# Kernel tuning notes

Measured on AMD Instinct MI355X. Metric: run time of the kernel, lower is better.

## Reference

```python
import jax, jax.numpy as jnp
import numpy as np

B, N, QDIM = 2, 4096, 768
H, D = 8, 64  # num_head, head_dim; inner_dim = 512
INNER = H * D


def setup_inputs() -> dict:
    key = jax.random.key(0)
    ks = jax.random.split(key, 6)
    s = lambda fan_in: 1.0 / np.sqrt(fan_in)
    return {
        "x": jax.random.normal(ks[0], (B, N, QDIM), dtype=jnp.float32),
        "Wq": jax.random.normal(ks[1], (QDIM, INNER), dtype=jnp.float32) * s(QDIM),
        "Wk": jax.random.normal(ks[2], (QDIM, INNER), dtype=jnp.float32) * s(QDIM),
        "Wv": jax.random.normal(ks[3], (QDIM, INNER), dtype=jnp.float32) * s(QDIM),
        "Wout": jax.random.normal(ks[4], (INNER, QDIM), dtype=jnp.float32) * s(INNER),
        "b_out": jnp.zeros((QDIM,), dtype=jnp.float32),
    }


def reference(x, Wq, Wk, Wv, Wout, b_out):
    # x: [b, n, q_dim]; self-attention (kv = x), no mask, dropout = 0 (eval).
    scale = D ** -0.5
    # project and split heads: [b, n, h*d] -> [b, h, n, d]
    def heads(t):
        b, n, _ = t.shape
        return t.reshape(b, n, H, D).transpose(0, 2, 1, 3)
    q = heads(x @ Wq)
    k = heads(x @ Wk)
    v = heads(x @ Wv)
    qk = jnp.einsum("bhid,bhjd->bhij", q, k) * scale  # [b, h, n, n] -- O(n^2) matrix
    attn = jax.nn.softmax(qk, axis=-1)
    out = jnp.einsum("bhij,bhjd->bhid", attn, v)  # [b, h, n, d]
    out = out.transpose(0, 2, 1, 3).reshape(x.shape[0], x.shape[1], INNER)
    return out @ Wout + b_out
```

## Files before the change

kernel.cpp:

```cpp
#include <hip/hip_runtime.h>
#include <cstdint>
#include <cstddef>


typedef __attribute__((ext_vector_type(8))) short short8;
typedef __attribute__((ext_vector_type(4))) float f32x4;

__device__ __forceinline__ unsigned short f2bf(float f) {
  unsigned int u = __float_as_uint(f);
  u = (u + 0x7fffu + ((u >> 16) & 1u)) >> 16;
  return (unsigned short)u;
}

__device__ __forceinline__ float fast_exp2(float x) {
#if __has_builtin(__builtin_amdgcn_exp2f)
  return __builtin_amdgcn_exp2f(x);
#else
  return __expf(x * 0.69314718055994531f);
#endif
}

__device__ __forceinline__ void gld16(const void* g, void* l) {
  __builtin_amdgcn_global_load_lds(
      (__attribute__((address_space(1))) void*)const_cast<void*>(g),
      (__attribute__((address_space(3))) void*)l, 16, 0, 0);
}


__global__ __launch_bounds__(256) void cvt_x_k(const float* __restrict__ x,
                                               unsigned short* __restrict__ xb) {
  const size_t i = ((size_t)blockIdx.x * 256 + threadIdx.x) * 4;
  const float4 v = *(const float4*)(x + i);
  ushort4 u;
  u.x = f2bf(v.x); u.y = f2bf(v.y); u.z = f2bf(v.z); u.w = f2bf(v.w);
  *(ushort4*)(xb + i) = u;
}

__global__ __launch_bounds__(256) void transpose_w_k(
    const float* __restrict__ Wq, const float* __restrict__ Wk,
    const float* __restrict__ Wv, const float* __restrict__ Wout,
    unsigned short* __restrict__ Wt,
    unsigned short* __restrict__ WoT)
{
  __shared__ float t[32][33];
  const int z = blockIdx.z;
  const float* src = (z == 0) ? Wq : (z == 1) ? Wk : (z == 2) ? Wv : Wout;
  const int R = (z < 3) ? 768 : 512, C = (z < 3) ? 512 : 768;
  unsigned short* dst = (z < 3) ? (Wt + (size_t)z * 393216) : WoT;
  const int tx = threadIdx.x & 31, ty = threadIdx.x >> 5;
  const int c0 = blockIdx.x * 32, r0 = blockIdx.y * 32;
  if (c0 >= C || r0 >= R) return;
#pragma unroll
  for (int k = 0; k < 4; ++k)
    t[ty + 8 * k][tx] = src[(size_t)(r0 + ty + 8 * k) * C + c0 + tx];
  __syncthreads();
#pragma unroll
  for (int k = 0; k < 4; ++k)
    dst[(size_t)(c0 + ty + 8 * k) * R + r0 + tx] = f2bf(t[tx][ty + 8 * k]);
}


__global__ __launch_bounds__(256) void gemm_qkv_k(
    const unsigned short* __restrict__ A,
    const unsigned short* __restrict__ Wt,
    unsigned short* __restrict__ qb, unsigned short* __restrict__ kb,
    unsigned short* __restrict__ vtb) {
  __shared__ __align__(16) short Al[4096];
  __shared__ __align__(16) short Bl[4096];
  const int tid = threadIdx.x;
  const int w = tid >> 6, lane = tid & 63, quad = lane >> 4, l15 = lane & 15;
  const int wy = w >> 1, wx = w & 1;
  const int m0 = blockIdx.x * 128, n0 = blockIdx.y * 128;
  const int z = blockIdx.z;
  const unsigned short* Bt = Wt + (size_t)z * (512 * 768);

  f32x4 acc[4][4];
#pragma unroll
  for (int i = 0; i < 4; ++i)
#pragma unroll
    for (int j = 0; j < 4; ++j) acc[i][j] = (f32x4){0.f, 0.f, 0.f, 0.f};

  for (int k0 = 0; k0 < 768; k0 += 32) {
    __syncthreads();
#pragma unroll
    for (int s = 0; s < 2; ++s) {
      const int t = s * 256 + tid;
      gld16(A + (size_t)(m0 + (t >> 2)) * 768 + k0 + (t & 3) * 8,
            Al + s * 2048 + w * 512);
      gld16(Bt + (size_t)(n0 + (t >> 2)) * 768 + k0 + (t & 3) * 8,
            Bl + s * 2048 + w * 512);
    }
    __syncthreads();
    short8 af[4], bf[4];
#pragma unroll
    for (int i = 0; i < 4; ++i) {
      af[i] = *(const short8*)(Al + (wy * 64 + i * 16 + l15) * 32 + quad * 8);
      bf[i] = *(const short8*)(Bl + (wx * 64 + i * 16 + l15) * 32 + quad * 8);
    }
    if (z == 2) {
#pragma unroll
      for (int i = 0; i < 4; ++i)
#pragma unroll
        for (int j = 0; j < 4; ++j)
          acc[i][j] = __builtin_amdgcn_mfma_f32_16x16x32_bf16(af[i], bf[j], acc[i][j], 0, 0, 0);
    } else {
#pragma unroll
      for (int i = 0; i < 4; ++i)
#pragma unroll
        for (int j = 0; j < 4; ++j)
          acc[i][j] = __builtin_amdgcn_mfma_f32_16x16x32_bf16(bf[i], af[j], acc[i][j], 0, 0, 0);
    }
  }

  if (z == 2) {
#pragma unroll
    for (int i = 0; i < 4; ++i) {
#pragma unroll
      for (int j = 0; j < 4; ++j) {
        const int m0r = m0 + wy * 64 + i * 16 + quad * 4;
        const int n = n0 + wx * 64 + j * 16 + l15;
        const int b = m0r >> 12, nseq0 = m0r & 4095;
        const int h = n >> 6, d = n & 63;
        ushort4 u;
        u.x = f2bf(acc[i][j][0]); u.y = f2bf(acc[i][j][1]);
        u.z = f2bf(acc[i][j][2]); u.w = f2bf(acc[i][j][3]);
        *(ushort4*)(vtb + (size_t)((b * 8 + h) * 64 + d) * 4096 + nseq0) = u;
      }
    }
  } else {
    const float qs = 0.18033688011112042f;
#pragma unroll
    for (int i = 0; i < 4; ++i) {
#pragma unroll
      for (int j = 0; j < 4; ++j) {
        const int n0r = n0 + wx * 64 + i * 16 + quad * 4;
        const int m = m0 + wy * 64 + j * 16 + l15;
        const int b = m >> 12, nseq = m & 4095;
        const int h = n0r >> 6, d0 = n0r & 63;
        ushort4 u;
        if (z == 0) {
          u.x = f2bf(acc[i][j][0] * qs); u.y = f2bf(acc[i][j][1] * qs);
          u.z = f2bf(acc[i][j][2] * qs); u.w = f2bf(acc[i][j][3] * qs);
          *(ushort4*)(qb + (size_t)((b * 8 + h) * 4096 + nseq) * 64 + d0) = u;
        } else {
          u.x = f2bf(acc[i][j][0]); u.y = f2bf(acc[i][j][1]);
          u.z = f2bf(acc[i][j][2]); u.w = f2bf(acc[i][j][3]);
          *(ushort4*)(kb + (size_t)((b * 8 + h) * 4096 + nseq) * 64 + d0) = u;
        }
      }
    }
  }
}


__global__ __launch_bounds__(256) void attn_k(
    const unsigned short* __restrict__ qb,
    const unsigned short* __restrict__ kb,
    const unsigned short* __restrict__ vtb,
    unsigned short* __restrict__ ob) {
  __shared__ __align__(16) char smem[65536];
  short* Kl = (short*)smem;
  short* Vl = (short*)(smem + 16384);
  short* Pl = (short*)(smem + 32768);

  const int tid = threadIdx.x;
  const int w = tid >> 6, lane = tid & 63, quad = lane >> 4, l15 = lane & 15;
  const int g = w >> 1, wq = w & 1;
  const int bh = blockIdx.y;
  const int q0 = blockIdx.x * 128;
  const unsigned short* qbase = qb + (size_t)bh * 4096 * 64;
  const unsigned short* kbase = kb + (size_t)bh * 4096 * 64;
  const unsigned short* vbase = vtb + (size_t)bh * 64 * 4096;
  short* pw = Pl + w * 4096;
  short* KlG = Kl + g * 4096;
  short* VlG = Vl + g * 4096;
  const int jbase = g * 2048;
  const int e8 = l15 & 7;

  short8 qf[4][2];
#pragma unroll
  for (int qh = 0; qh < 4; ++qh) {
    const int qrow = q0 + wq * 64 + qh * 16 + l15;
    qf[qh][0] = *(const short8*)(qbase + (size_t)qrow * 64 + quad * 8);
    qf[qh][1] = *(const short8*)(qbase + (size_t)qrow * 64 + 32 + quad * 8);
  }

  const short one_bf = (short)0x3F80;
  const short8 vones = {one_bf, one_bf, one_bf, one_bf,
                        one_bf, one_bf, one_bf, one_bf};

  f32x4 Oacc[4][4];
#pragma unroll
  for (int qh = 0; qh < 4; ++qh)
#pragma unroll
    for (int nf = 0; nf < 4; ++nf) Oacc[qh][nf] = (f32x4){0.f, 0.f, 0.f, 0.f};
  f32x4 Lacc[4];
#pragma unroll
  for (int qh = 0; qh < 4; ++qh) Lacc[qh] = (f32x4){0.f, 0.f, 0.f, 0.f};

  for (int j0 = 0; j0 < 2048; j0 += 64) {
    const int jj = jbase + j0;
    __syncthreads();
#pragma unroll
    for (int c = 0; c < 2; ++c) {
#pragma unroll
      for (int hf = 0; hf < 2; ++hf) {
        const int row = wq * 32 + hf * 16;
        gld16(kbase + (size_t)(jj + row + (lane >> 2)) * 64 + c * 32 + (lane & 3) * 8,
              KlG + (c * 64 + row) * 32);
        gld16(vbase + (size_t)(row + (lane >> 2)) * 4096 + jj + c * 32 + (lane & 3) * 8,
              VlG + (c * 64 + row) * 32);
      }
    }
    __syncthreads();

#pragma unroll
    for (int kt = 0; kt < 4; ++kt) {
      const short8 ka0 = *(const short8*)(KlG + (0 * 64 + kt * 16 + l15) * 32 + quad * 8);
      const short8 ka1 = *(const short8*)(KlG + (1 * 64 + kt * 16 + l15) * 32 + quad * 8);
#pragma unroll
      for (int qh = 0; qh < 4; ++qh) {
        f32x4 st = (f32x4){0.f, 0.f, 0.f, 0.f};
        st = __builtin_amdgcn_mfma_f32_16x16x32_bf16(ka0, qf[qh][0], st, 0, 0, 0);
        st = __builtin_amdgcn_mfma_f32_16x16x32_bf16(ka1, qf[qh][1], st, 0, 0, 0);
        const unsigned int u0 = __float_as_uint(fast_exp2(st[0]));
        const unsigned int u1 = __float_as_uint(fast_exp2(st[1]));
        const unsigned int u2 = __float_as_uint(fast_exp2(st[2]));
        const unsigned int u3 = __float_as_uint(fast_exp2(st[3]));
        uint2 pd;
        pd.x = (u1 & 0xFFFF0000u) | (u0 >> 16);
        pd.y = (u3 & 0xFFFF0000u) | (u2 >> 16);
        *(uint2*)(pw + (qh * 16 + l15) * 64 +
                  (((2 * kt + (quad >> 1)) ^ e8) * 8 + (quad & 1) * 4)) = pd;
      }
    }

    asm volatile("s_waitcnt lgkmcnt(0)" ::: "memory");

#pragma unroll
    for (int c = 0; c < 2; ++c) {
      short8 pa[4];
#pragma unroll
      for (int qh = 0; qh < 4; ++qh)
        pa[qh] = *(const short8*)(pw + (qh * 16 + l15) * 64 +
                                  ((4 * c + quad) ^ e8) * 8);
#pragma unroll
      for (int nf = 0; nf < 4; ++nf) {
        const short8 vb = *(const short8*)(VlG + (c * 64 + nf * 16 + l15) * 32 + quad * 8);
#pragma unroll
        for (int qh = 0; qh < 4; ++qh)
          Oacc[qh][nf] = __builtin_amdgcn_mfma_f32_16x16x32_bf16(
              pa[qh], vb, Oacc[qh][nf], 0, 0, 0);
      }
#pragma unroll
      for (int qh = 0; qh < 4; ++qh)
        Lacc[qh] = __builtin_amdgcn_mfma_f32_16x16x32_bf16(pa[qh], vones, Lacc[qh], 0, 0, 0);
    }
  }

  __syncthreads();
  float* Ox = (float*)smem;
  float* Lx = (float*)(smem + 33280);
  if (g == 1) {
#pragma unroll
    for (int qh = 0; qh < 4; ++qh)
#pragma unroll
      for (int r = 0; r < 4; ++r) {
        const int rl = wq * 64 + qh * 16 + quad * 4 + r;
        Lx[rl] = Lacc[qh][r];
#pragma unroll
        for (int nf = 0; nf < 4; ++nf)
          Ox[rl * 65 + nf * 16 + l15] = Oacc[qh][nf][r];
      }
  }
  __syncthreads();
  if (g == 0) {
    const int b = bh >> 3, h = bh & 7;
#pragma unroll
    for (int qh = 0; qh < 4; ++qh)
#pragma unroll
      for (int r = 0; r < 4; ++r) {
        const int rl = wq * 64 + qh * 16 + quad * 4 + r;
        const float inv = 1.0f / (Lacc[qh][r] + Lx[rl]);
        const int row = q0 + rl;
#pragma unroll
        for (int nf = 0; nf < 4; ++nf)
          ob[(size_t)(b * 4096 + row) * 512 + h * 64 + nf * 16 + l15] =
              f2bf((Oacc[qh][nf][r] + Ox[rl * 65 + nf * 16 + l15]) * inv);
      }
  }
}


__global__ __launch_bounds__(256) void gemm_out_k(
    const unsigned short* __restrict__ A,
    const unsigned short* __restrict__ Bt,
    const float* __restrict__ bias, float* __restrict__ out) {
  __shared__ __align__(16) short Al[4096];
  __shared__ __align__(16) short Bl[2048];
  const int tid = threadIdx.x;
  const int w = tid >> 6, lane = tid & 63, quad = lane >> 4, l15 = lane & 15;
  const int m0 = blockIdx.x * 128, n0 = blockIdx.y * 64;

  f32x4 acc[2][4];
#pragma unroll
  for (int i = 0; i < 2; ++i)
#pragma unroll
    for (int j = 0; j < 4; ++j) acc[i][j] = (f32x4){0.f, 0.f, 0.f, 0.f};

  for (int k0 = 0; k0 < 512; k0 += 32) {
    __syncthreads();
#pragma unroll
    for (int s = 0; s < 2; ++s) {
      const int t = s * 256 + tid;
      gld16(A + (size_t)(m0 + (t >> 2)) * 512 + k0 + (t & 3) * 8,
            Al + s * 2048 + w * 512);
    }
    gld16(Bt + (size_t)(n0 + (tid >> 2)) * 512 + k0 + (tid & 3) * 8,
          Bl + w * 512);
    __syncthreads();
    short8 af[2], bf[4];
#pragma unroll
    for (int i = 0; i < 2; ++i)
      af[i] = *(const short8*)(Al + (w * 32 + i * 16 + l15) * 32 + quad * 8);
#pragma unroll
    for (int j = 0; j < 4; ++j)
      bf[j] = *(const short8*)(Bl + (j * 16 + l15) * 32 + quad * 8);
#pragma unroll
    for (int i = 0; i < 2; ++i)
#pragma unroll
      for (int j = 0; j < 4; ++j)
        acc[i][j] = __builtin_amdgcn_mfma_f32_16x16x32_bf16(bf[j], af[i], acc[i][j], 0, 0, 0);
  }

#pragma unroll
  for (int i = 0; i < 2; ++i) {
#pragma unroll
    for (int j = 0; j < 4; ++j) {
      const int col0 = n0 + j * 16 + quad * 4;
      const int m = m0 + w * 32 + i * 16 + l15;
      const float4 b4 = *(const float4*)(bias + col0);
      float4 o;
      o.x = acc[i][j][0] + b4.x; o.y = acc[i][j][1] + b4.y;
      o.z = acc[i][j][2] + b4.z; o.w = acc[i][j][3] + b4.w;
      *(float4*)(out + (size_t)m * 768 + col0) = o;
    }
  }
}


extern "C" void kernel_launch(void* const* d_in, const int* in_sizes, int n_in,
                              void* d_out, int out_size, void* d_ws, size_t ws_size,
                              hipStream_t stream) {
  const float* x    = (const float*)d_in[0];
  const float* Wq   = (const float*)d_in[1];
  const float* Wk   = (const float*)d_in[2];
  const float* Wv   = (const float*)d_in[3];
  const float* Wout = (const float*)d_in[4];
  const float* bout = (const float*)d_in[5];
  float* out = (float*)d_out;
  char* ws = (char*)d_ws;

  unsigned short* xb  = (unsigned short*)(ws);
  unsigned short* Wt  = (unsigned short*)(ws + 12582912);
  unsigned short* WoT = (unsigned short*)(ws + 14942208);
  unsigned short* qb  = (unsigned short*)(ws + 15728640);
  unsigned short* kb  = (unsigned short*)(ws + 24117248);
  unsigned short* vtb = (unsigned short*)(ws + 32505856);
  unsigned short* ob  = (unsigned short*)(ws + 40894464);

  cvt_x_k<<<6144, 256, 0, stream>>>(x, xb);
  transpose_w_k<<<dim3(24, 24, 4), 256, 0, stream>>>(Wq, Wk, Wv, Wout, Wt, WoT);
  gemm_qkv_k<<<dim3(64, 4, 3), 256, 0, stream>>>(xb, Wt, qb, kb, vtb);
  attn_k<<<dim3(32, 16), 256, 0, stream>>>(qb, kb, vtb, ob);
  gemm_out_k<<<dim3(64, 12), 256, 0, stream>>>(ob, WoT, bout, out);
}
```

Before: 241.2 us.

## Rewrite attention inner loop with 32x32 MFMA and register-resident P via lane shuffles

Switches the attention kernel from 16x16x32 to 32x32x16 bf16 MFMA. It loads K and V fragments directly from global memory into registers instead of staging them through LDS with barriers. The exponentiated scores are packed to bf16 and rearranged across half-waves with shuffles, so they feed the PV MFMA without an LDS round trip. The row sum is now computed with scalar adds rather than an extra MFMA against a ones vector, and blocks are remapped so neighbouring blocks share heads for L2 locality. This removes the per-tile syncthreads and LDS traffic, but every wave now reads K/V from global/L2 on its own and register pressure rises.

New measurement: 274.4 us. 1.14x slower.

```diff
diff --git a/kernel.cpp b/kernel.cpp
--- a/kernel.cpp
+++ b/kernel.cpp
@@ -5,11 +5,17 @@
 
 typedef __attribute__((ext_vector_type(8))) short short8;
 typedef __attribute__((ext_vector_type(4))) float f32x4;
+typedef __attribute__((ext_vector_type(16))) float f32x16;
+typedef __attribute__((ext_vector_type(4))) unsigned int uint4v;
 
 __device__ __forceinline__ unsigned short f2bf(float f) {
   unsigned int u = __float_as_uint(f);
   u = (u + 0x7fffu + ((u >> 16) & 1u)) >> 16;
   return (unsigned short)u;
+}
+
+__device__ __forceinline__ unsigned int packbf2(float lo, float hi) {
+  return (unsigned int)f2bf(lo) | ((unsigned int)f2bf(hi) << 16);
 }
 
 __device__ __forceinline__ float fast_exp2(float x) {
@@ -158,135 +164,140 @@
     const unsigned short* __restrict__ kb,
     const unsigned short* __restrict__ vtb,
     unsigned short* __restrict__ ob) {
-  __shared__ __align__(16) char smem[65536];
-  short* Kl = (short*)smem;
-  short* Vl = (short*)(smem + 16384);
-  short* Pl = (short*)(smem + 32768);
-
+  __shared__ __align__(16) char smem[34816];
   const int tid = threadIdx.x;
-  const int w = tid >> 6, lane = tid & 63, quad = lane >> 4, l15 = lane & 15;
+  const int w = tid >> 6, lane = tid & 63;
+  const int l31 = lane & 31, hi = lane >> 5;
   const int g = w >> 1, wq = w & 1;
-  const int bh = blockIdx.y;
-  const int q0 = blockIdx.x * 128;
-  const unsigned short* qbase = qb + (size_t)bh * 4096 * 64;
-  const unsigned short* kbase = kb + (size_t)bh * 4096 * 64;
-  const unsigned short* vbase = vtb + (size_t)bh * 64 * 4096;
-  short* pw = Pl + w * 4096;
-  short* KlG = Kl + g * 4096;
-  short* VlG = Vl + g * 4096;
+
+  const int L = blockIdx.x + 32 * blockIdx.y;
+  const int bh = ((L & 7) << 1) | ((L >> 3) & 1);
+  const int q0 = (L >> 4) << 7;
+
+  const unsigned short* qbase = qb + (size_t)bh * (4096 * 64);
+  const unsigned short* kbase = kb + (size_t)bh * (4096 * 64);
+  const unsigned short* vbase = vtb + (size_t)bh * (64 * 4096);
+
+  short8 qf[2][4];
+#pragma unroll
+  for (int qs = 0; qs < 2; ++qs) {
+    const int qrow = q0 + wq * 64 + qs * 32 + l31;
+#pragma unroll
+    for (int c = 0; c < 4; ++c)
+      qf[qs][c] = *(const short8*)(qbase + (size_t)qrow * 64 + c * 16 + hi * 8);
+  }
+
+  f32x16 Oacc[2][2];
+#pragma unroll
+  for (int qs = 0; qs < 2; ++qs)
+#pragma unroll
+    for (int dt = 0; dt < 2; ++dt)
+#pragma unroll
+      for (int r = 0; r < 16; ++r) Oacc[qs][dt][r] = 0.f;
+  float lsum[2] = {0.f, 0.f};
+
   const int jbase = g * 2048;
-  const int e8 = l15 & 7;
-
-  short8 qf[4][2];
-#pragma unroll
-  for (int qh = 0; qh < 4; ++qh) {
-    const int qrow = q0 + wq * 64 + qh * 16 + l15;
-    qf[qh][0] = *(const short8*)(qbase + (size_t)qrow * 64 + quad * 8);
-    qf[qh][1] = *(const short8*)(qbase + (size_t)qrow * 64 + 32 + quad * 8);
-  }
-
-  const short one_bf = (short)0x3F80;
-  const short8 vones = {one_bf, one_bf, one_bf, one_bf,
-                        one_bf, one_bf, one_bf, one_bf};
-
-  f32x4 Oacc[4][4];
-#pragma unroll
-  for (int qh = 0; qh < 4; ++qh)
-#pragma unroll
-    for (int nf = 0; nf < 4; ++nf) Oacc[qh][nf] = (f32x4){0.f, 0.f, 0.f, 0.f};
-  f32x4 Lacc[4];
-#pragma unroll
-  for (int qh = 0; qh < 4; ++qh) Lacc[qh] = (f32x4){0.f, 0.f, 0.f, 0.f};
 
   for (int j0 = 0; j0 < 2048; j0 += 64) {
     const int jj = jbase + j0;
-    __syncthreads();
-#pragma unroll
-    for (int c = 0; c < 2; ++c) {
-#pragma unroll
-      for (int hf = 0; hf < 2; ++hf) {
-        const int row = wq * 32 + hf * 16;
-        gld16(kbase + (size_t)(jj + row + (lane >> 2)) * 64 + c * 32 + (lane & 3) * 8,
-              KlG + (c * 64 + row) * 32);
-        gld16(vbase + (size_t)(row + (lane >> 2)) * 4096 + jj + c * 32 + (lane & 3) * 8,
-              VlG + (c * 64 + row) * 32);
+
+#pragma unroll
+    for (int kt = 0; kt < 2; ++kt) {
+      short8 kf[4];
+#pragma unroll
+      for (int c = 0; c < 4; ++c)
+        kf[c] = *(const short8*)(kbase + (size_t)(jj + kt * 32 + l31) * 64 + c * 16 + hi * 8);
+      short8 vfr[2][2];
+#pragma unroll
+      for (int dt = 0; dt < 2; ++dt)
+#pragma unroll
+        for (int kc = 0; kc < 2; ++kc)
+          vfr[dt][kc] = *(const short8*)(vbase + (size_t)(dt * 32 + l31) * 4096 +
+                                         jj + kt * 32 + kc * 16 + hi * 8);
+
+      uint4v pa[2][2];
+#pragma unroll
+      for (int qs = 0; qs < 2; ++qs) {
+        f32x16 s;
+#pragma unroll
+        for (int r = 0; r < 16; ++r) s[r] = 0.f;
+#pragma unroll
+        for (int c = 0; c < 4; ++c)
+          s = __builtin_amdgcn_mfma_f32_32x32x16_bf16(kf[c], qf[qs][c], s, 0, 0, 0);
+
+        float e[16];
+#pragma unroll
+        for (int r = 0; r < 16; ++r) e[r] = fast_exp2(s[r]);
+        lsum[qs] += (((e[0] + e[1]) + (e[2] + e[3])) + ((e[4] + e[5]) + (e[6] + e[7]))) +
+                    (((e[8] + e[9]) + (e[10] + e[11])) + ((e[12] + e[13]) + (e[14] + e[15])));
+
+        unsigned int wv[8];
+#pragma unroll
+        for (int g2 = 0; g2 < 4; ++g2)
+#pragma unroll
+          for (int p = 0; p < 2; ++p)
+            wv[g2 * 2 + p] = packbf2(e[4 * g2 + 2 * p], e[4 * g2 + 2 * p + 1]);
+
+        const unsigned int s0 = hi ? wv[0] : wv[2];
+        const unsigned int s1 = hi ? wv[1] : wv[3];
+        const unsigned int s2 = hi ? wv[4] : wv[6];
+        const unsigned int s3 = hi ? wv[5] : wv[7];
+        const unsigned int x0 = __shfl_xor(s0, 32, 64);
+        const unsigned int x1 = __shfl_xor(s1, 32, 64);
+        const unsigned int x2 = __shfl_xor(s2, 32, 64);
+        const unsigned int x3 = __shfl_xor(s3, 32, 64);
+        pa[qs][0] = (uint4v){hi ? x0 : wv[0], hi ? x1 : wv[1],
+                             hi ? wv[2] : x0, hi ? wv[3] : x1};
+        pa[qs][1] = (uint4v){hi ? x2 : wv[4], hi ? x3 : wv[5],
+                             hi ? wv[6] : x2, hi ? wv[7] : x3};
       }
-    }
-    __syncthreads();
-
-#pragma unroll
-    for (int kt = 0; kt < 4; ++kt) {
-      const short8 ka0 = *(const short8*)(KlG + (0 * 64 + kt * 16 + l15) * 32 + quad * 8);
-      const short8 ka1 = *(const short8*)(KlG + (1 * 64 + kt * 16 + l15) * 32 + quad * 8);
-#pragma unroll
-      for (int qh = 0; qh < 4; ++qh) {
-        f32x4 st = (f32x4){0.f, 0.f, 0.f, 0.f};
-        st = __builtin_amdgcn_mfma_f32_16x16x32_bf16(ka0, qf[qh][0], st, 0, 0, 0);
-        st = __builtin_amdgcn_mfma_f32_16x16x32_bf16(ka1, qf[qh][1], st, 0, 0, 0);
-        const unsigned int u0 = __float_as_uint(fast_exp2(st[0]));
-        const unsigned int u1 = __float_as_uint(fast_exp2(st[1]));
-        const unsigned int u2 = __float_as_uint(fast_exp2(st[2]));
-        const unsigned int u3 = __float_as_uint(fast_exp2(st[3]));
-        uint2 pd;
-        pd.x = (u1 & 0xFFFF0000u) | (u0 >> 16);
-        pd.y = (u3 & 0xFFFF0000u) | (u2 >> 16);
-        *(uint2*)(pw + (qh * 16 + l15) * 64 +
-                  (((2 * kt + (quad >> 1)) ^ e8) * 8 + (quad & 1) * 4)) = pd;
-      }
-    }
-
-    asm volatile("s_waitcnt lgkmcnt(0)" ::: "memory");
-
-#pragma unroll
-    for (int c = 0; c < 2; ++c) {
-      short8 pa[4];
-#pragma unroll
-      for (int qh = 0; qh < 4; ++qh)
-        pa[qh] = *(const short8*)(pw + (qh * 16 + l15) * 64 +
-                                  ((4 * c + quad) ^ e8) * 8);
-#pragma unroll
-      for (int nf = 0; nf < 4; ++nf) {
-        const short8 vb = *(const short8*)(VlG + (c * 64 + nf * 16 + l15) * 32 + quad * 8);
-#pragma unroll
-        for (int qh = 0; qh < 4; ++qh)
-          Oacc[qh][nf] = __builtin_amdgcn_mfma_f32_16x16x32_bf16(
-              pa[qh], vb, Oacc[qh][nf], 0, 0, 0);
-      }
-#pragma unroll
-      for (int qh = 0; qh < 4; ++qh)
-        Lacc[qh] = __builtin_amdgcn_mfma_f32_16x16x32_bf16(pa[qh], vones, Lacc[qh], 0, 0, 0);
-    }
-  }
+
+#pragma unroll
+      for (int dt = 0; dt < 2; ++dt)
+#pragma unroll
+        for (int kc = 0; kc < 2; ++kc)
+#pragma unroll
+          for (int qs = 0; qs < 2; ++qs)
+            Oacc[qs][dt] = __builtin_amdgcn_mfma_f32_32x32x16_bf16(
+                __builtin_bit_cast(short8, pa[qs][kc]), vfr[dt][kc], Oacc[qs][dt], 0, 0, 0);
+    }
+  }
+
+  float lt[2];
+#pragma unroll
+  for (int qs = 0; qs < 2; ++qs)
+    lt[qs] = lsum[qs] + __shfl_xor(lsum[qs], 32, 64);
 
   __syncthreads();
   float* Ox = (float*)smem;
-  float* Lx = (float*)(smem + 33280);
+  float* Lx = (float*)(smem + 33792);
+#pragma unroll
+  for (int qs = 0; qs < 2; ++qs)
+    Lx[g * 128 + wq * 64 + qs * 32 + l31] = lt[qs];
   if (g == 1) {
 #pragma unroll
-    for (int qh = 0; qh < 4; ++qh)
-#pragma unroll
-      for (int r = 0; r < 4; ++r) {
-        const int rl = wq * 64 + qh * 16 + quad * 4 + r;
-        Lx[rl] = Lacc[qh][r];
-#pragma unroll
-        for (int nf = 0; nf < 4; ++nf)
-          Ox[rl * 65 + nf * 16 + l15] = Oacc[qh][nf][r];
-      }
+    for (int qs = 0; qs < 2; ++qs)
+#pragma unroll
+      for (int dt = 0; dt < 2; ++dt)
+#pragma unroll
+        for (int r = 0; r < 16; ++r) {
+          const int row = wq * 64 + qs * 32 + (r & 3) + 8 * (r >> 2) + 4 * hi;
+          Ox[row * 66 + dt * 32 + l31] = Oacc[qs][dt][r];
+        }
   }
   __syncthreads();
   if (g == 0) {
     const int b = bh >> 3, h = bh & 7;
 #pragma unroll
-    for (int qh = 0; qh < 4; ++qh)
-#pragma unroll
-      for (int r = 0; r < 4; ++r) {
-        const int rl = wq * 64 + qh * 16 + quad * 4 + r;
-        const float inv = 1.0f / (Lacc[qh][r] + Lx[rl]);
-        const int row = q0 + rl;
-#pragma unroll
-        for (int nf = 0; nf < 4; ++nf)
-          ob[(size_t)(b * 4096 + row) * 512 + h * 64 + nf * 16 + l15] =
-              f2bf((Oacc[qh][nf][r] + Ox[rl * 65 + nf * 16 + l15]) * inv);
+    for (int qs = 0; qs < 2; ++qs)
+#pragma unroll
+      for (int r = 0; r < 16; ++r) {
+        const int row = wq * 64 + qs * 32 + (r & 3) + 8 * (r >> 2) + 4 * hi;
+        const float inv = 1.0f / (Lx[row] + Lx[128 + row]);
+#pragma unroll
+        for (int dt = 0; dt < 2; ++dt)
+          ob[(size_t)(b * 4096 + q0 + row) * 512 + h * 64 + dt * 32 + l31] =
+              f2bf((Oacc[qs][dt][r] + Ox[row * 66 + dt * 32 + l31]) * inv);
       }
   }
 }
```
